# Kernel tuning notes

Hardware: AMD Instinct MI355X
Metric: run time of the kernel (lower is better)

Reference implementation:

```python
import jax, jax.numpy as jnp
import numpy as np

DIM_MODEL = 1024
DIM_LLM = 4096
HEAD_NUM = 16
DIM_KEYS = DIM_MODEL // HEAD_NUM  # 64


def setup_inputs() -> dict:
    key = jax.random.key(0)
    ks = jax.random.split(key, 11)
    B, P, V = 8, 256, 8192
    s_q = 1.0 / np.sqrt(DIM_MODEL)
    s_l = 1.0 / np.sqrt(DIM_LLM)
    s_d = 1.0 / np.sqrt(DIM_MODEL)
    return {
        "query": jax.random.normal(ks[0], (B, P, DIM_MODEL), dtype=jnp.float32),
        "key": jax.random.normal(ks[1], (V, DIM_LLM), dtype=jnp.float32),
        "value": jax.random.normal(ks[2], (V, DIM_LLM), dtype=jnp.float32),
        "Wq": jax.random.normal(ks[3], (DIM_MODEL, DIM_MODEL), dtype=jnp.float32) * s_q,
        "bq": jnp.zeros((DIM_MODEL,), dtype=jnp.float32),
        "Wk": jax.random.normal(ks[4], (DIM_LLM, DIM_MODEL), dtype=jnp.float32) * s_l,
        "bk": jnp.zeros((DIM_MODEL,), dtype=jnp.float32),
        "Wv": jax.random.normal(ks[5], (DIM_LLM, DIM_MODEL), dtype=jnp.float32) * s_l,
        "bv": jnp.zeros((DIM_MODEL,), dtype=jnp.float32),
        "Wo": jax.random.normal(ks[6], (DIM_MODEL, DIM_LLM), dtype=jnp.float32) * s_d,
        "bo": jnp.zeros((DIM_LLM,), dtype=jnp.float32),
    }


def reference(query, key, value, Wq, bq, Wk, bk, Wv, bv, Wo, bo):
    B, P, _ = query.shape
    V = key.shape[0]
    # projections
    q = (query @ Wq + bq).reshape(B, P, HEAD_NUM, DIM_KEYS)        # [b,p,h,k]
    k = (key @ Wk + bk).reshape(V, HEAD_NUM, DIM_KEYS)             # [v,h,k]
    v = (value @ Wv + bv).reshape(V, HEAD_NUM, DIM_KEYS)           # [v,h,k]
    scale = 1.0 / DIM_KEYS  # NOTE: original uses 1/d_k, not 1/sqrt(d_k)
    scores = jnp.einsum('bphk,vhk->bhpv', q, k)                    # [b,h,p,v]
    A = jax.nn.softmax(scale * scores, axis=-1)                    # dropout is identity in eval
    mapped = jnp.einsum('bhpv,vhk->bphk', A, v)                    # [b,p,h,k]
    mapped = mapped.reshape(B, P, HEAD_NUM * DIM_KEYS)
    return mapped @ Wo + bo                                        # [b,p,dim_llm]
```

## Files before the change

kernel.cpp:

```cpp
#include <hip/hip_runtime.h>


typedef __attribute__((ext_vector_type(8)))  short          short8;
typedef __attribute__((ext_vector_type(4)))  float          f32x4;
typedef __attribute__((ext_vector_type(16))) float          f32x16;
typedef __attribute__((ext_vector_type(8)))  unsigned short ushort8;
typedef __attribute__((ext_vector_type(4)))  unsigned int   uint4v;

__device__ __forceinline__ unsigned short f2bf(float f) {
    unsigned int u = __builtin_bit_cast(unsigned int, f);
    u += 0x7fffu + ((u >> 16) & 1u);
    return (unsigned short)(u >> 16);
}

__device__ __forceinline__ void gld_lds16(const ushort* g, ushort* l) {
    __builtin_amdgcn_global_load_lds(
        (const __attribute__((address_space(1))) void*)g,
        (__attribute__((address_space(3))) void*)l, 16, 0, 0);
}

__global__ __launch_bounds__(256) void conv_f32_bf16(
    const float* __restrict__ in, ushort* __restrict__ out, int n)
{
    int i = (blockIdx.x * 256 + threadIdx.x) * 8;
    if (i >= n) return;
    float4 a = *(const float4*)(in + i);
    float4 b = *(const float4*)(in + i + 4);
    ushort8 o = {f2bf(a.x), f2bf(a.y), f2bf(a.z), f2bf(a.w),
                 f2bf(b.x), f2bf(b.y), f2bf(b.z), f2bf(b.w)};
    *(ushort8*)(out + i) = o;
}

__global__ __launch_bounds__(256) void transconv(
    const float* __restrict__ in, ushort* __restrict__ out, int R, int C)
{
    __shared__ float t[32][33];
    const int tx = threadIdx.x & 31, ty = threadIdx.x >> 5;
    const int bx = blockIdx.x, by = blockIdx.y;
#pragma unroll
    for (int i = 0; i < 4; ++i)
        t[ty + 8 * i][tx] = in[(size_t)(by * 32 + ty + 8 * i) * C + bx * 32 + tx];
    __syncthreads();
#pragma unroll
    for (int i = 0; i < 4; ++i)
        out[(size_t)(bx * 32 + ty + 8 * i) * R + by * 32 + tx] = f2bf(t[tx][ty + 8 * i]);
}

template<int OUT_BF16, int BIAS_ROW>
__global__ __launch_bounds__(256) void gemm_bt(
    const ushort* __restrict__ A, const ushort* __restrict__ BT,
    const float* __restrict__ bias, void* __restrict__ Cout,
    int M, int N, int K, float oscale)
{
    __shared__ ushort As[128 * 32];
    __shared__ ushort Bs[128 * 32];
    const int tid = threadIdx.x;
    const int w = tid >> 6, lane = tid & 63;
    const int m = lane & 15, quad = lane >> 4;
    const int wr = w >> 1, wc = w & 1;
    const int bx = blockIdx.x, by = blockIdx.y;

    f32x4 acc[4][4];
#pragma unroll
    for (int i = 0; i < 4; ++i)
#pragma unroll
        for (int j = 0; j < 4; ++j)
#pragma unroll
            for (int r = 0; r < 4; ++r) acc[i][j][r] = 0.f;

    const int r_i = lane >> 2;
    const int ccl = (lane & 3) ^ ((lane >> 2) & 3) ^ quad;
    const ushort* Ag = A  + (size_t)(by * 128 + w * 32 + r_i) * K + ccl * 8;
    const ushort* Bg = BT + (size_t)(bx * 128 + w * 32 + r_i) * K + ccl * 8;
    ushort* AsW = As + w * 1024;
    ushort* BsW = Bs + w * 1024;
    const size_t rowstep = (size_t)16 * K;

    const int phys = (quad ^ (m & 3) ^ (m >> 2)) * 8;
    int aoff[4], boff[4];
#pragma unroll
    for (int i = 0; i < 4; ++i) {
        aoff[i] = (wr * 64 + i * 16 + m) * 32 + phys;
        boff[i] = (wc * 64 + i * 16 + m) * 32 + phys;
    }

    const int kIters = K >> 5;
    for (int kt = 0; kt < kIters; ++kt) {
        __syncthreads();
        gld_lds16(Ag, AsW);
        gld_lds16(Ag + rowstep, AsW + 512);
        gld_lds16(Bg, BsW);
        gld_lds16(Bg + rowstep, BsW + 512);
        Ag += 32; Bg += 32;
        __syncthreads();
        short8 af[4], bf[4];
#pragma unroll
        for (int i = 0; i < 4; ++i) af[i] = *(const short8*)(As + aoff[i]);
#pragma unroll
        for (int i = 0; i < 4; ++i) bf[i] = *(const short8*)(Bs + boff[i]);
#pragma unroll
        for (int i = 0; i < 4; ++i)
#pragma unroll
            for (int j = 0; j < 4; ++j)
                acc[i][j] = __builtin_amdgcn_mfma_f32_16x16x32_bf16(
                    af[i], bf[j], acc[i][j], 0, 0, 0);
    }

    const int row0 = by * 128 + wr * 64;
    const int col0 = bx * 128 + wc * 64;
#pragma unroll
    for (int i = 0; i < 4; ++i) {
#pragma unroll
        for (int j = 0; j < 4; ++j) {
            const int c = col0 + j * 16 + m;
            float bcol = BIAS_ROW ? 0.f : bias[c];
#pragma unroll
            for (int r = 0; r < 4; ++r) {
                const int rw = row0 + i * 16 + quad * 4 + r;
                float v = acc[i][j][r] + (BIAS_ROW ? bias[rw] : bcol);
                v *= oscale;
                if (OUT_BF16)
                    ((ushort*)Cout)[(size_t)rw * N + c] = f2bf(v);
                else
                    ((float*)Cout)[(size_t)rw * N + c] = v;
            }
        }
    }
}

__global__ __launch_bounds__(512, 4) void attn_mfma(
    const ushort* __restrict__ qb, const ushort* __restrict__ kb,
    const ushort* __restrict__ vT, ushort* __restrict__ mappedb)
{
    __shared__ ushort Qs[64 * 64];
    __shared__ ushort Ks[128 * 64];
    __shared__ ushort Vs[64 * 128];

    const int tid = threadIdx.x;
    const int w = tid >> 6, lane = tid & 63;
    const int l31 = lane & 31, l5 = lane >> 5, quad = lane >> 4;
    const int wp = w >> 2, wv = w & 3;
    const int idx = blockIdx.x;
    const int pt = idx & 3, h = (idx >> 2) & 15, b = idx >> 6;
    const int pbase = b * 256 + pt * 64;

    const int c8 = lane & 7, r8 = lane >> 3, c16 = lane & 15;

    {
        const ushort* g = qb + (size_t)(pbase + w * 8 + r8) * 1024 + h * 64 + c8 * 8;
        gld_lds16(g, Qs + w * 512);
    }
    __syncthreads();
    short8 qf[4];
#pragma unroll
    for (int ks = 0; ks < 4; ++ks)
        qf[ks] = *(const short8*)(Qs + (wp * 32 + l31) * 64 + ks * 16 + l5 * 8);

    f32x16 o[2];
#pragma unroll
    for (int dt = 0; dt < 2; ++dt)
#pragma unroll
        for (int r = 0; r < 16; ++r) o[dt][r] = 0.f;
    float lpart = 0.f;

    const int ccK = c8 ^ r8;

    for (int vt = 0; vt < 8192; vt += 128) {
        __syncthreads();
#pragma unroll
        for (int i = 0; i < 2; ++i) {
            const int t = w * 2 + i;
            const ushort* gk = kb + (size_t)(vt + t * 8 + r8) * 1024 + h * 64 + ccK * 8;
            gld_lds16(gk, Ks + t * 512);
            const int d_l = t * 4 + quad;
            const int ccV = c16 ^ (d_l & 15);
            const ushort* gv = vT + (size_t)(h * 64 + d_l) * 8192 + vt + ccV * 8;
            gld_lds16(gv, Vs + t * 512);
        }
        __syncthreads();

        f32x16 st;
#pragma unroll
        for (int r = 0; r < 16; ++r) st[r] = 0.f;
        {
            const int row = (wv * 32 + l31) * 64;
            const int sw = l31 & 7;
            __builtin_amdgcn_s_setprio(1);
#pragma unroll
            for (int ks = 0; ks < 4; ++ks) {
                const int ph = ((ks * 2 + l5) ^ sw) * 8;
                short8 kf = *(const short8*)(Ks + row + ph);
                st = __builtin_amdgcn_mfma_f32_32x32x16_bf16(kf, qf[ks], st, 0, 0, 0);
            }
            __builtin_amdgcn_s_setprio(0);
        }

#pragma unroll
        for (int k4 = 0; k4 < 2; ++k4) {
            float e[8];
#pragma unroll
            for (int t = 0; t < 8; ++t) e[t] = exp2f(st[k4 * 8 + t]);
            lpart += ((e[0] + e[1]) + (e[2] + e[3])) + ((e[4] + e[5]) + (e[6] + e[7]));
            unsigned int a0, a1, b0, b1;
            asm("v_cvt_pk_bf16_f32 %0, %1, %2" : "=v"(a0) : "v"(e[0]), "v"(e[1]));
            asm("v_cvt_pk_bf16_f32 %0, %1, %2" : "=v"(a1) : "v"(e[2]), "v"(e[3]));
            asm("v_cvt_pk_bf16_f32 %0, %1, %2" : "=v"(b0) : "v"(e[4]), "v"(e[5]));
            asm("v_cvt_pk_bf16_f32 %0, %1, %2" : "=v"(b1) : "v"(e[6]), "v"(e[7]));
            asm("v_permlane32_swap_b32 %0, %1" : "+v"(a0), "+v"(b0));
            asm("v_permlane32_swap_b32 %0, %1" : "+v"(a1), "+v"(b1));
            uint4v pfw = {a0, a1, b0, b1};
            short8 pf = __builtin_bit_cast(short8, pfw);
            const int k8 = wv * 2 + k4;
            __builtin_amdgcn_s_setprio(1);
#pragma unroll
            for (int dt = 0; dt < 2; ++dt) {
                const int d_l = dt * 32 + l31;
                const int ph = ((k8 * 2 + l5) ^ (d_l & 15)) * 8;
                short8 vf = *(const short8*)(Vs + d_l * 128 + ph);
                o[dt] = __builtin_amdgcn_mfma_f32_32x32x16_bf16(pf, vf, o[dt], 0, 0, 0);
            }
            __builtin_amdgcn_s_setprio(0);
        }
    }

    float* RedA = (float*)Ks;
    float* RedB = (float*)Vs;
    float* Lq   = (float*)Qs;
    Lq[w * 64 + lane] = lpart;
    __syncthreads();
    if (wv >= 2) {
        float* R = (wv == 2) ? RedA : RedB;
#pragma unroll
        for (int dt = 0; dt < 2; ++dt)
#pragma unroll
            for (int r = 0; r < 16; ++r)
                R[wp * 2048 + (dt * 16 + r) * 64 + lane] = o[dt][r];
    }
    __syncthreads();
    if (wv < 2) {
        float* R = (wv == 0) ? RedA : RedB;
#pragma unroll
        for (int dt = 0; dt < 2; ++dt)
#pragma unroll
            for (int r = 0; r < 16; ++r)
                o[dt][r] += R[wp * 2048 + (dt * 16 + r) * 64 + lane];
    }
    __syncthreads();
    if (wv == 1) {
#pragma unroll
        for (int dt = 0; dt < 2; ++dt)
#pragma unroll
            for (int r = 0; r < 16; ++r)
                RedA[wp * 2048 + (dt * 16 + r) * 64 + lane] = o[dt][r];
    }
    __syncthreads();
    if (wv == 0) {
#pragma unroll
        for (int dt = 0; dt < 2; ++dt)
#pragma unroll
            for (int r = 0; r < 16; ++r)
                o[dt][r] += RedA[wp * 2048 + (dt * 16 + r) * 64 + lane];
        float lsum = (Lq[(wp * 4 + 0) * 64 + lane] + Lq[(wp * 4 + 1) * 64 + lane])
                   + (Lq[(wp * 4 + 2) * 64 + lane] + Lq[(wp * 4 + 3) * 64 + lane]);

        float lfull = lsum + __shfl_xor(lsum, 32, 64);
        float rinv = 1.0f / lfull;
#pragma unroll
        for (int r = 0; r < 16; ++r) {
            const int poff = (r & 3) + 8 * (r >> 2) + 4 * l5;
            const float sc = __shfl(rinv, poff, 64);
            const size_t grow = (size_t)(pbase + wp * 32 + poff) * 1024;
#pragma unroll
            for (int dt = 0; dt < 2; ++dt)
                mappedb[grow + h * 64 + dt * 32 + l31] = f2bf(o[dt][r] * sc);
        }
    }
}

extern "C" void kernel_launch(void* const* d_in, const int* in_sizes, int n_in,
                              void* d_out, int out_size, void* d_ws, size_t ws_size,
                              hipStream_t stream)
{
    const float* query = (const float*)d_in[0];
    const float* key   = (const float*)d_in[1];
    const float* value = (const float*)d_in[2];
    const float* Wq    = (const float*)d_in[3];
    const float* bq    = (const float*)d_in[4];
    const float* Wk    = (const float*)d_in[5];
    const float* bk    = (const float*)d_in[6];
    const float* Wv    = (const float*)d_in[7];
    const float* bv    = (const float*)d_in[8];
    const float* Wo    = (const float*)d_in[9];
    const float* bo    = (const float*)d_in[10];
    float* out = (float*)d_out;

    char* ws = (char*)d_ws;
    ushort* tmpb    = (ushort*)ws;
    ushort* wslot   = (ushort*)(ws + (64ull << 20));
    ushort* queryb  = (ushort*)(ws + (72ull << 20));
    ushort* qb      = (ushort*)(ws + (76ull << 20));
    ushort* mappedb = (ushort*)ws;
    ushort* kb      = (ushort*)d_out;
    ushort* vT      = (ushort*)((char*)d_out + (16ull << 20));

    const float QSCALE = 1.4426950408889634f / 64.0f;

    conv_f32_bf16<<<16384, 256, 0, stream>>>(key, tmpb, 8192 * 4096);
    transconv<<<dim3(32, 128), 256, 0, stream>>>(Wk, wslot, 4096, 1024);
    gemm_bt<1, 0><<<dim3(8, 64), 256, 0, stream>>>(tmpb, wslot, bk, kb,
                                                   8192, 1024, 4096, 1.0f);
    conv_f32_bf16<<<16384, 256, 0, stream>>>(value, tmpb, 8192 * 4096);
    transconv<<<dim3(32, 128), 256, 0, stream>>>(Wv, wslot, 4096, 1024);
    gemm_bt<1, 1><<<dim3(64, 8), 256, 0, stream>>>(wslot, tmpb, bv, vT,
                                                   1024, 8192, 4096, 1.0f);
    conv_f32_bf16<<<1024, 256, 0, stream>>>(query, queryb, 2048 * 1024);
    transconv<<<dim3(32, 32), 256, 0, stream>>>(Wq, wslot, 1024, 1024);
    gemm_bt<1, 0><<<dim3(8, 16), 256, 0, stream>>>(queryb, wslot, bq, qb,
                                                   2048, 1024, 1024, QSCALE);
    attn_mfma<<<512, 512, 0, stream>>>(qb, kb, vT, mappedb);
    transconv<<<dim3(128, 32), 256, 0, stream>>>(Wo, wslot, 1024, 4096);
    gemm_bt<0, 0><<<dim3(32, 16), 256, 0, stream>>>(mappedb, wslot, bo, out,
                                                    2048, 4096, 1024, 1.0f);
}
```

Before: 713.0 us.

## Double-buffer K/V tiles in attention kernel to overlap loads with MFMA

Doubles the LDS K and V tile buffers and prefetches tile t+1 into the alternate buffer while tile t is computed. Partial vmcnt waits plus raw s_barrier replace the two full __syncthreads per iteration. The intent is to hide global-to-LDS load latency behind the score and PV MFMAs. The cost is doubled LDS use (about 72KB per block), which may cut occupancy under launch_bounds(512,4). The final iteration also issues a wasted wraparound prefetch of tile 0.

```diff
diff --git a/kernel.cpp b/kernel.cpp
--- a/kernel.cpp
+++ b/kernel.cpp
@@ -133,8 +133,8 @@
     const ushort* __restrict__ vT, ushort* __restrict__ mappedb)
 {
     __shared__ ushort Qs[64 * 64];
-    __shared__ ushort Ks[128 * 64];
-    __shared__ ushort Vs[64 * 128];
+    __shared__ ushort Ks[2][128 * 64];
+    __shared__ ushort Vs[2][64 * 128];
 
     const int tid = threadIdx.x;
     const int w = tid >> 6, lane = tid & 63;
@@ -145,12 +145,26 @@
     const int pbase = b * 256 + pt * 64;
 
     const int c8 = lane & 7, r8 = lane >> 3, c16 = lane & 15;
+    const int ccK = c8 ^ r8;
+
+    const int t0 = w * 2, t1 = w * 2 + 1;
+    const ushort* gk0 = kb + (size_t)(t0 * 8 + r8) * 1024 + h * 64 + ccK * 8;
+    const ushort* gk1 = kb + (size_t)(t1 * 8 + r8) * 1024 + h * 64 + ccK * 8;
+    const int d0 = t0 * 4 + quad, d1 = t1 * 4 + quad;
+    const ushort* gv0 = vT + (size_t)(h * 64 + d0) * 8192 + ((c16 ^ (d0 & 15)) * 8);
+    const ushort* gv1 = vT + (size_t)(h * 64 + d1) * 8192 + ((c16 ^ (d1 & 15)) * 8);
 
     {
         const ushort* g = qb + (size_t)(pbase + w * 8 + r8) * 1024 + h * 64 + c8 * 8;
         gld_lds16(g, Qs + w * 512);
     }
-    __syncthreads();
+    gld_lds16(gk0, Ks[0] + t0 * 512);
+    gld_lds16(gk1, Ks[0] + t1 * 512);
+    gld_lds16(gv0, Vs[0] + t0 * 512);
+    gld_lds16(gv1, Vs[0] + t1 * 512);
+    asm volatile("s_waitcnt vmcnt(4)" ::: "memory");
+    __builtin_amdgcn_s_barrier();
+    __builtin_amdgcn_sched_barrier(0);
     short8 qf[4];
 #pragma unroll
     for (int ks = 0; ks < 4; ++ks)
@@ -163,21 +177,24 @@
         for (int r = 0; r < 16; ++r) o[dt][r] = 0.f;
     float lpart = 0.f;
 
-    const int ccK = c8 ^ r8;
-
-    for (int vt = 0; vt < 8192; vt += 128) {
-        __syncthreads();
-#pragma unroll
-        for (int i = 0; i < 2; ++i) {
-            const int t = w * 2 + i;
-            const ushort* gk = kb + (size_t)(vt + t * 8 + r8) * 1024 + h * 64 + ccK * 8;
-            gld_lds16(gk, Ks + t * 512);
-            const int d_l = t * 4 + quad;
-            const int ccV = c16 ^ (d_l & 15);
-            const ushort* gv = vT + (size_t)(h * 64 + d_l) * 8192 + vt + ccV * 8;
-            gld_lds16(gv, Vs + t * 512);
-        }
-        __syncthreads();
+    for (int t = 0; t < 64; ++t) {
+        const int cur = t & 1;
+        {
+            const size_t koff = (size_t)(((t + 1) & 63) * 128) * 1024;
+            const size_t voff = (size_t)(((t + 1) & 63) * 128);
+            ushort* KsN = Ks[cur ^ 1];
+            ushort* VsN = Vs[cur ^ 1];
+            gld_lds16(gk0 + koff, KsN + t0 * 512);
+            gld_lds16(gk1 + koff, KsN + t1 * 512);
+            gld_lds16(gv0 + voff, VsN + t0 * 512);
+            gld_lds16(gv1 + voff, VsN + t1 * 512);
+        }
+        asm volatile("s_waitcnt vmcnt(4)" ::: "memory");
+        __builtin_amdgcn_s_barrier();
+        __builtin_amdgcn_sched_barrier(0);
+
+        const ushort* KsC = Ks[cur];
+        const ushort* VsC = Vs[cur];
 
         f32x16 st;
 #pragma unroll
@@ -189,7 +206,7 @@
 #pragma unroll
             for (int ks = 0; ks < 4; ++ks) {
                 const int ph = ((ks * 2 + l5) ^ sw) * 8;
-                short8 kf = *(const short8*)(Ks + row + ph);
+                short8 kf = *(const short8*)(KsC + row + ph);
                 st = __builtin_amdgcn_mfma_f32_32x32x16_bf16(kf, qf[ks], st, 0, 0, 0);
             }
             __builtin_amdgcn_s_setprio(0);
@@ -199,7 +216,7 @@
         for (int k4 = 0; k4 < 2; ++k4) {
             float e[8];
 #pragma unroll
-            for (int t = 0; t < 8; ++t) e[t] = exp2f(st[k4 * 8 + t]);
+            for (int tt = 0; tt < 8; ++tt) e[tt] = exp2f(st[k4 * 8 + tt]);
             lpart += ((e[0] + e[1]) + (e[2] + e[3])) + ((e[4] + e[5]) + (e[6] + e[7]));
             unsigned int a0, a1, b0, b1;
             asm("v_cvt_pk_bf16_f32 %0, %1, %2" : "=v"(a0) : "v"(e[0]), "v"(e[1]));
@@ -216,15 +233,17 @@
             for (int dt = 0; dt < 2; ++dt) {
                 const int d_l = dt * 32 + l31;
                 const int ph = ((k8 * 2 + l5) ^ (d_l & 15)) * 8;
-                short8 vf = *(const short8*)(Vs + d_l * 128 + ph);
+                short8 vf = *(const short8*)(VsC + d_l * 128 + ph);
                 o[dt] = __builtin_amdgcn_mfma_f32_32x32x16_bf16(pf, vf, o[dt], 0, 0, 0);
             }
             __builtin_amdgcn_s_setprio(0);
         }
-    }
-
-    float* RedA = (float*)Ks;
-    float* RedB = (float*)Vs;
+        __builtin_amdgcn_sched_barrier(0);
+        __builtin_amdgcn_s_barrier();
+    }
+
+    float* RedA = (float*)Ks[0];
+    float* RedB = (float*)Vs[0];
     float* Lq   = (float*)Qs;
     Lq[w * 64 + lane] = lpart;
     __syncthreads();
```

New measurement: 707.7 us. About the same (-0.8%).
